# Kernel optimization log

Measured on AMD Instinct MI355X. Metric: run time of the kernel, lower is better.

The kernel has to match this reference:

```python
import jax, jax.numpy as jnp
import numpy as np
import math

B, D, NH, HD, FF, P, IMG = 4, 768, 12, 64, 3072, 16, 256
L = (IMG // P) ** 2      # 256 tokens
PD = P * P * 3           # 768 patch dim
GRID = IMG // P          # 16


def setup_inputs() -> dict:
    key = jax.random.key(0)
    ks = iter(jax.random.split(key, 80))
    def nrm(shape, s=0.02):
        return jax.random.normal(next(ks), shape, jnp.float32) * s
    return {
        "x": jax.random.normal(next(ks), (B, 3, IMG, IMG), jnp.float32),
        "pe_norm_w": jnp.ones((PD,), jnp.float32),
        "pe_proj_w": nrm((PD, D)),
        "pe_proj_b": jnp.zeros((D,), jnp.float32),
        "pe_norm_out_w": jnp.ones((D,), jnp.float32),
        "pos_embed": nrm((1, L, D)),
        "in_attn_norm_w": jnp.ones((6, D), jnp.float32),
        "in_qkv_w": nrm((6, D, 3 * D)),
        "in_out_w": nrm((6, D, D)),
        "in_ff_norm_w": jnp.ones((6, D), jnp.float32),
        "in_w1": nrm((6, D, 2 * FF)),
        "in_w2": nrm((6, FF, D)),
        "mid_attn_norm_w": jnp.ones((3, D), jnp.float32),
        "mid_qkv_w": nrm((3, D, 3 * D)),
        "mid_out_w": nrm((3, D, D)),
        "mid_ff_norm_w": jnp.ones((3, D), jnp.float32),
        "mid_w1": nrm((3, D, 2 * FF)),
        "mid_w2": nrm((3, FF, D)),
        "out_skip_w": nrm((2 * D, D)),
        "out_skip_b": jnp.zeros((D,), jnp.float32),
        "out_attn_norm_w": jnp.ones((D,), jnp.float32),
        "out_qkv_w": nrm((D, 3 * D)),
        "out_out_w": nrm((D, D)),
        "out_ff_norm_w": jnp.ones((D,), jnp.float32),
        "out_w1": nrm((D, 2 * FF)),
        "out_w2": nrm((FF, D)),
        "final_norm_w": jnp.ones((D,), jnp.float32),
        "ol_proj_w": nrm((D, PD)),
        "ol_proj_b": jnp.zeros((PD,), jnp.float32),
        "rb_conv_in_w": nrm((128, 3, 3, 3), 0.1),
        "rb_gn_w": jnp.ones((5, 128), jnp.float32),
        "rb_gn_b": jnp.zeros((5, 128), jnp.float32),
        "rb_conv1_w": nrm((128, 1, 5, 5), 0.1),
        "rb_conv2_w": nrm((128, 1, 5, 5), 0.1),
        "head_conv_w": nrm((1, 128, 3, 3), 0.1),
    }


def _mish(x):
    return x * jnp.tanh(jax.nn.softplus(x))


def _rms(x, w, eps=1e-5):
    return x * jax.lax.rsqrt(jnp.mean(x * x, axis=-1, keepdims=True) + eps) * w


def _attn(x, qkv_w, out_w):
    b, l, _ = x.shape
    q, k, v = jnp.split(x @ qkv_w, 3, axis=-1)
    s = 1.0 / math.sqrt(HD)  # applied to BOTH q and k, as in source
    q = (q * s).reshape(b, l, NH, HD)
    k = (k * s).reshape(b, l, NH, HD)
    v = v.reshape(b, l, NH, HD)
    logits = jnp.einsum('bqhd,bkhd->bhqk', q, k).astype(jnp.float32)
    w = jax.nn.softmax(logits, axis=-1).astype(x.dtype)
    o = jnp.einsum('bhqk,bkhd->bqhd', w, v).reshape(b, l, NH * HD)
    return o @ out_w


def _ff(x, w1, w2):
    a, g = jnp.split(x @ w1, 2, axis=-1)
    return (_mish(a) * g) @ w2


def _block(x, an, qkv, ow, fn, w1, w2):
    x = x + _attn(_rms(x, an), qkv, ow)
    x = x + _ff(_rms(x, fn), w1, w2)
    return x


def _gn(x, w, b, groups=8, eps=1e-5):
    bb, c, h, ww = x.shape
    xg = x.reshape(bb, groups, c // groups, h, ww)
    m = jnp.mean(xg, axis=(2, 3, 4), keepdims=True)
    v = jnp.var(xg, axis=(2, 3, 4), keepdims=True)
    xn = ((xg - m) * jax.lax.rsqrt(v + eps)).reshape(bb, c, h, ww)
    return xn * w[:, None, None] + b[:, None, None]


def _conv(x, w, pad, dil=1, groups=1):
    xp = jnp.pad(x, ((0, 0), (0, 0), (pad, pad), (pad, pad)), mode='reflect')
    return jax.lax.conv_general_dilated(
        xp, w, window_strides=(1, 1), padding='VALID', rhs_dilation=(dil, dil),
        feature_group_count=groups, dimension_numbers=('NCHW', 'OIHW', 'NCHW'))


def _forward(x, pe_norm_w, pe_proj_w, pe_proj_b, pe_norm_out_w, pos_embed,
             in_attn_norm_w, in_qkv_w, in_out_w, in_ff_norm_w, in_w1, in_w2,
             mid_attn_norm_w, mid_qkv_w, mid_out_w, mid_ff_norm_w, mid_w1, mid_w2,
             out_skip_w, out_skip_b, out_attn_norm_w, out_qkv_w, out_out_w,
             out_ff_norm_w, out_w1, out_w2, final_norm_w, ol_proj_w, ol_proj_b,
             rb_conv_in_w, rb_gn_w, rb_gn_b, rb_conv1_w, rb_conv2_w, head_conv_w):
    b = x.shape[0]
    # PatchEmbed: b c (h p1) (w p2) -> b (h w) (p1 p2 c)
    t = x.reshape(b, 3, GRID, P, GRID, P).transpose(0, 2, 4, 3, 5, 1).reshape(b, L, PD)
    t = _rms(t, pe_norm_w)
    t = t @ pe_proj_w + pe_proj_b
    t = _rms(t, pe_norm_out_w)
    t = t + pos_embed
    # U-ViT trunk: 6 in blocks (skips saved), 3 middle, 1 out block (source typo -> single out block)
    skips = []
    for i in range(6):
        t = _block(t, in_attn_norm_w[i], in_qkv_w[i], in_out_w[i],
                   in_ff_norm_w[i], in_w1[i], in_w2[i])
        skips.append(t)
    for i in range(3):
        t = _block(t, mid_attn_norm_w[i], mid_qkv_w[i], mid_out_w[i],
                   mid_ff_norm_w[i], mid_w1[i], mid_w2[i])
    t = jnp.concatenate([t, skips[-1]], axis=-1) @ out_skip_w + out_skip_b
    t = _block(t, out_attn_norm_w, out_qkv_w, out_out_w, out_ff_norm_w, out_w1, out_w2)
    t = _rms(t, final_norm_w)
    # OutBlock: proj, dropout(eval=identity), unpatchify to b 3 256 256
    t = t @ ol_proj_w + ol_proj_b
    img = t.reshape(b, GRID, GRID, P, P, 3).transpose(0, 5, 1, 3, 2, 4).reshape(b, 3, IMG, IMG)
    # ResNetBlock(128)
    h = _conv(img, rb_conv_in_w, 1)
    h = _mish(_gn(h, rb_gn_w[0], rb_gn_b[0]))
    res = h
    h = _mish(_gn(_conv(h, rb_conv1_w, 2, 1, 128), rb_gn_w[1], rb_gn_b[1]))
    h = res + h
    h = _mish(_gn(h, rb_gn_w[2], rb_gn_b[2]))
    res = h
    h = _mish(_gn(_conv(h, rb_conv2_w, 6, 3, 128), rb_gn_w[3], rb_gn_b[3]))
    h = res + h
    h = _mish(_gn(h, rb_gn_w[4], rb_gn_b[4]))
    return _conv(h, head_conv_w, 1)  # [B, 1, 256, 256]


def reference(x, pe_norm_w, pe_proj_w, pe_proj_b, pe_norm_out_w, pos_embed,
              in_attn_norm_w, in_qkv_w, in_out_w, in_ff_norm_w, in_w1, in_w2,
              mid_attn_norm_w, mid_qkv_w, mid_out_w, mid_ff_norm_w, mid_w1, mid_w2,
              out_skip_w, out_skip_b, out_attn_norm_w, out_qkv_w, out_out_w,
              out_ff_norm_w, out_w1, out_w2, final_norm_w, ol_proj_w, ol_proj_b,
              rb_conv_in_w, rb_gn_w, rb_gn_b, rb_conv1_w, rb_conv2_w, head_conv_w):
    return _forward(x, pe_norm_w, pe_proj_w, pe_proj_b, pe_norm_out_w, pos_embed,
                    in_attn_norm_w, in_qkv_w, in_out_w, in_ff_norm_w, in_w1, in_w2,
                    mid_attn_norm_w, mid_qkv_w, mid_out_w, mid_ff_norm_w, mid_w1, mid_w2,
                    out_skip_w, out_skip_b, out_attn_norm_w, out_qkv_w, out_out_w,
                    out_ff_norm_w, out_w1, out_w2, final_norm_w, ol_proj_w, ol_proj_b,
                    rb_conv_in_w, rb_gn_w, rb_gn_b, rb_conv1_w, rb_conv2_w, head_conv_w)
```

## Files before the change

### kernel.cpp

```cpp
#include <hip/hip_runtime.h>
#include <math.h>

#define B_ 4
#define D_ 768
#define NH_ 12
#define HD_ 64
#define FF_ 3072
#define L_ 256
#define PD_ 768
#define GRID_ 16
#define P_ 16
#define IMG_ 256
#define M_ (B_*L_)
#define NCONV_ (B_*128*IMG_*IMG_)

typedef __attribute__((ext_vector_type(8))) short short8;
typedef __attribute__((ext_vector_type(4))) float f32x4;
typedef __attribute__((ext_vector_type(4))) unsigned short us4;
typedef __attribute__((ext_vector_type(8))) unsigned short us8;
typedef unsigned short ushort_t;

__device__ __forceinline__ float mishf(float x){
    float e = __expf(x);
    float u = (1.f + e) * (1.f + e);
    return x * (1.f - 2.f / (u + 1.f));
}

__device__ __forceinline__ int refl(int i, int n){
    if (i < 0) i = -i;
    if (i >= n) i = 2*n - 2 - i;
    return i;
}

__device__ __forceinline__ ushort_t f2bf(float f){
    unsigned int u = __float_as_uint(f);
    unsigned int r = (u + 0x7FFFu + ((u >> 16) & 1u)) >> 16;
    return (ushort_t)r;
}
__device__ __forceinline__ float bf2f(ushort_t u){
    return __uint_as_float(((unsigned int)u) << 16);
}

__device__ __forceinline__ void gl16(const void* g, void* l){
    __builtin_amdgcn_global_load_lds(
        (const __attribute__((address_space(1))) unsigned int*)g,
        (__attribute__((address_space(3))) unsigned int*)l, 16, 0, 0);
}

__device__ __forceinline__ void block_red2(float& s, float& q){
    #pragma unroll
    for (int o = 32; o > 0; o >>= 1){ s += __shfl_down(s, o); q += __shfl_down(q, o); }
    __shared__ float r1[4], r2[4];
    int tid = threadIdx.x;
    if ((tid & 63) == 0){ r1[tid>>6] = s; r2[tid>>6] = q; }
    __syncthreads();
    if (tid == 0){ s = r1[0]+r1[1]+r1[2]+r1[3]; q = r2[0]+r2[1]+r2[2]+r2[3]; }
    __syncthreads();
}

__global__ __launch_bounds__(256) void k_patchify(const float* __restrict__ x, float* __restrict__ t){
    int idx = blockIdx.x*256 + threadIdx.x;
    int d = idx % PD_; int l = (idx/PD_) % L_; int b = idx/(PD_*L_);
    int c = d % 3; int p = d / 3; int p1 = p / P_; int p2 = p % P_;
    int gh = l / GRID_; int gw = l % GRID_;
    int sy = gh*P_ + p1, sx = gw*P_ + p2;
    t[idx] = x[(((size_t)b*3 + c)*IMG_ + sy)*IMG_ + sx];
}

__global__ __launch_bounds__(256) void k_wt(const float* __restrict__ b0, const float* __restrict__ b1,
                                            const float* __restrict__ b2, int n0, int n1,
                                            ushort_t* __restrict__ dst, int K, int N){
    int z = blockIdx.z;
    size_t sz = (size_t)K * N;
    const float* src = (z < n0) ? b0 + (size_t)z*sz
                     : (z < n0+n1) ? b1 + (size_t)(z-n0)*sz
                     : b2 + (size_t)(z-n0-n1)*sz;
    ushort_t* out = dst + (size_t)z*sz;
    __shared__ float ld[32][33];
    int k0 = blockIdx.y*32, nc0 = blockIdx.x*32;
    int tid = threadIdx.x;
    int c = tid & 31, r8 = tid >> 5;
    #pragma unroll
    for (int i = 0; i < 4; ++i){
        int k = r8 + i*8;
        ld[k][c] = src[(size_t)(k0+k)*N + nc0 + c];
    }
    __syncthreads();
    #pragma unroll
    for (int i = 0; i < 4; ++i){
        int n = r8 + i*8;
        out[(size_t)(nc0+n)*K + k0 + c] = f2bf(ld[c][n]);
    }
}

template<bool OUT_BF>
__global__ __launch_bounds__(256) void k_rms(const float* __restrict__ x, const float* __restrict__ w,
                                             const float* __restrict__ addv, void* __restrict__ yv){
    int row = blockIdx.x;
    const float* xr = x + (size_t)row * D_;
    float s = 0.f;
    for (int i = threadIdx.x; i < D_; i += 256){ float v = xr[i]; s += v*v; }
    __shared__ float red[256];
    red[threadIdx.x] = s; __syncthreads();
    for (int o = 128; o > 0; o >>= 1){
        if (threadIdx.x < o) red[threadIdx.x] += red[threadIdx.x+o];
        __syncthreads();
    }
    float rstd = rsqrtf(red[0]/(float)D_ + 1e-5f);
    int l = row % L_;
    for (int i = threadIdx.x; i < D_; i += 256){
        float v = xr[i]*rstd*w[i];
        if (addv) v += addv[(size_t)l*D_ + i];
        if (OUT_BF) ((ushort_t*)yv)[(size_t)row*D_ + i] = f2bf(v);
        else        ((float*)yv)[(size_t)row*D_ + i] = v;
    }
}

__global__ __launch_bounds__(256) void k_skred_rms(const float* __restrict__ Pp, float* __restrict__ t,
                                                   const float* __restrict__ w, ushort_t* __restrict__ nb){
    int row = blockIdx.x;
    int tid = threadIdx.x;
    float v[3];
    float s = 0.f;
    #pragma unroll
    for (int i = 0; i < 3; ++i){
        int c = tid + i*256;
        size_t o = (size_t)row*D_ + c;
        float x = t[o] + Pp[o] + Pp[(size_t)M_*D_ + o];
        v[i] = x; s += x*x;
        t[o] = x;
    }
    #pragma unroll
    for (int o = 32; o > 0; o >>= 1) s += __shfl_down(s, o);
    __shared__ float r1[4];
    if ((tid & 63) == 0) r1[tid>>6] = s;
    __syncthreads();
    float tot = r1[0]+r1[1]+r1[2]+r1[3];
    float rstd = rsqrtf(tot*(1.f/768.f) + 1e-5f);
    if (w){
        #pragma unroll
        for (int i = 0; i < 3; ++i){
            int c = tid + i*256;
            nb[(size_t)row*D_ + c] = f2bf(v[i]*rstd*w[c]);
        }
    }
}

template<bool OBF, int SPLITK>
__global__ __launch_bounds__(256) void k_gemm(const ushort_t* __restrict__ A, const ushort_t* __restrict__ Wt,
                                              void* __restrict__ Cv, const float* __restrict__ bias,
                                              const float* __restrict__ res, int N, int K){
    __shared__ ushort_t As[2][64][32];
    __shared__ ushort_t Ws[2][64][32];
    int tid = threadIdx.x;
    int lane = tid & 63, wid = tid >> 6;
    int wr = wid >> 1, wc = wid & 1;
    int row0 = blockIdx.y * 64, col0 = blockIdx.x * 64;
    f32x4 acc[2][2];
    #pragma unroll
    for (int i = 0; i < 2; ++i)
        #pragma unroll
        for (int j = 0; j < 2; ++j) acc[i][j] = (f32x4){0.f,0.f,0.f,0.f};

    int lg = lane >> 4, lr = lane & 15;
    int kc = K / SPLITK;
    int k0 = (SPLITK > 1) ? blockIdx.z * kc : 0;
    int srow = wid*16 + (lane >> 2);
    int scol = (lane & 3) * 8;
    const ushort_t* gA = A  + (size_t)(row0 + srow)*K + k0 + scol;
    const ushort_t* gW = Wt + (size_t)(col0 + srow)*K + k0 + scol;
    ushort_t* lA0 = &As[0][wid*16][0];
    ushort_t* lA1 = &As[1][wid*16][0];
    ushort_t* lW0 = &Ws[0][wid*16][0];
    ushort_t* lW1 = &Ws[1][wid*16][0];

    for (int kt = 0; kt < kc; kt += 64){
        __syncthreads();
        gl16(gA + kt,      lA0);
        gl16(gA + kt + 32, lA1);
        gl16(gW + kt,      lW0);
        gl16(gW + kt + 32, lW1);
        __syncthreads();
        short8 a0[2], a1[2], b0[2], b1[2];
        #pragma unroll
        for (int i = 0; i < 2; ++i){
            a0[i] = *(const short8*)(&As[0][wr*32 + i*16 + lr][lg*8]);
            a1[i] = *(const short8*)(&As[1][wr*32 + i*16 + lr][lg*8]);
        }
        #pragma unroll
        for (int j = 0; j < 2; ++j){
            b0[j] = *(const short8*)(&Ws[0][wc*32 + j*16 + lr][lg*8]);
            b1[j] = *(const short8*)(&Ws[1][wc*32 + j*16 + lr][lg*8]);
        }
        #pragma unroll
        for (int i = 0; i < 2; ++i)
            #pragma unroll
            for (int j = 0; j < 2; ++j){
                acc[i][j] = __builtin_amdgcn_mfma_f32_16x16x32_bf16(a0[i], b0[j], acc[i][j], 0, 0, 0);
                acc[i][j] = __builtin_amdgcn_mfma_f32_16x16x32_bf16(a1[i], b1[j], acc[i][j], 0, 0, 0);
            }
    }
    if (SPLITK > 1){
        float* Pp = (float*)Cv + (size_t)blockIdx.z * M_ * N;
        #pragma unroll
        for (int i = 0; i < 2; ++i)
            #pragma unroll
            for (int j = 0; j < 2; ++j)
                #pragma unroll
                for (int q = 0; q < 4; ++q){
                    int m = row0 + wr*32 + i*16 + lg*4 + q;
                    int n = col0 + wc*32 + j*16 + lr;
                    Pp[(size_t)m*N + n] = acc[i][j][q];
                }
    } else {
        #pragma unroll
        for (int i = 0; i < 2; ++i)
            #pragma unroll
            for (int j = 0; j < 2; ++j)
                #pragma unroll
                for (int q = 0; q < 4; ++q){
                    int m = row0 + wr*32 + i*16 + lg*4 + q;
                    int n = col0 + wc*32 + j*16 + lr;
                    float v = acc[i][j][q];
                    if (bias) v += bias[n];
                    size_t o = (size_t)m*N + n;
                    if (OBF){
                        ((ushort_t*)Cv)[o] = f2bf(v);
                    } else {
                        if (res) v += res[o];
                        ((float*)Cv)[o] = v;
                    }
                }
    }
}

__global__ __launch_bounds__(256) void k_gemm_glu(const ushort_t* __restrict__ A, const ushort_t* __restrict__ Wt,
                                                  ushort_t* __restrict__ Cb, int K){
    __shared__ ushort_t As[2][64][32];
    __shared__ ushort_t Wa[2][64][32];
    __shared__ ushort_t Wg[2][64][32];
    int tid = threadIdx.x;
    int lane = tid & 63, wid = tid >> 6;
    int wr = wid >> 1, wc = wid & 1;
    int row0 = blockIdx.y * 64, col0 = blockIdx.x * 64;
    f32x4 aa[2][2], ag[2][2];
    #pragma unroll
    for (int i = 0; i < 2; ++i)
        #pragma unroll
        for (int j = 0; j < 2; ++j){ aa[i][j] = (f32x4){0.f,0.f,0.f,0.f}; ag[i][j] = (f32x4){0.f,0.f,0.f,0.f}; }

    int lg = lane >> 4, lr = lane & 15;
    int srow = wid*16 + (lane >> 2);
    int scol = (lane & 3) * 8;
    const ushort_t* gA  = A  + (size_t)(row0 + srow)*K + scol;
    const ushort_t* gWa = Wt + (size_t)(col0 + srow)*K + scol;
    const ushort_t* gWg = Wt + (size_t)(FF_ + col0 + srow)*K + scol;
    ushort_t* lA0 = &As[0][wid*16][0];  ushort_t* lA1 = &As[1][wid*16][0];
    ushort_t* la0 = &Wa[0][wid*16][0];  ushort_t* la1 = &Wa[1][wid*16][0];
    ushort_t* lg0 = &Wg[0][wid*16][0];  ushort_t* lg1 = &Wg[1][wid*16][0];

    for (int kt = 0; kt < K; kt += 64){
        __syncthreads();
        gl16(gA  + kt,      lA0);
        gl16(gA  + kt + 32, lA1);
        gl16(gWa + kt,      la0);
        gl16(gWa + kt + 32, la1);
        gl16(gWg + kt,      lg0);
        gl16(gWg + kt + 32, lg1);
        __syncthreads();
        short8 a0[2], a1[2], ba0[2], ba1[2], bg0[2], bg1[2];
        #pragma unroll
        for (int i = 0; i < 2; ++i){
            a0[i] = *(const short8*)(&As[0][wr*32 + i*16 + lr][lg*8]);
            a1[i] = *(const short8*)(&As[1][wr*32 + i*16 + lr][lg*8]);
        }
        #pragma unroll
        for (int j = 0; j < 2; ++j){
            ba0[j] = *(const short8*)(&Wa[0][wc*32 + j*16 + lr][lg*8]);
            ba1[j] = *(const short8*)(&Wa[1][wc*32 + j*16 + lr][lg*8]);
            bg0[j] = *(const short8*)(&Wg[0][wc*32 + j*16 + lr][lg*8]);
            bg1[j] = *(const short8*)(&Wg[1][wc*32 + j*16 + lr][lg*8]);
        }
        #pragma unroll
        for (int i = 0; i < 2; ++i)
            #pragma unroll
            for (int j = 0; j < 2; ++j){
                aa[i][j] = __builtin_amdgcn_mfma_f32_16x16x32_bf16(a0[i], ba0[j], aa[i][j], 0, 0, 0);
                aa[i][j] = __builtin_amdgcn_mfma_f32_16x16x32_bf16(a1[i], ba1[j], aa[i][j], 0, 0, 0);
                ag[i][j] = __builtin_amdgcn_mfma_f32_16x16x32_bf16(a0[i], bg0[j], ag[i][j], 0, 0, 0);
                ag[i][j] = __builtin_amdgcn_mfma_f32_16x16x32_bf16(a1[i], bg1[j], ag[i][j], 0, 0, 0);
            }
    }
    #pragma unroll
    for (int i = 0; i < 2; ++i)
        #pragma unroll
        for (int j = 0; j < 2; ++j)
            #pragma unroll
            for (int q = 0; q < 4; ++q){
                int m = row0 + wr*32 + i*16 + lg*4 + q;
                int n = col0 + wc*32 + j*16 + lr;
                Cb[(size_t)m*FF_ + n] = f2bf(mishf(aa[i][j][q]) * ag[i][j][q]);
            }
}

__global__ __launch_bounds__(256) void k_attn(const ushort_t* __restrict__ qkv, ushort_t* __restrict__ out){
    int qt = blockIdx.x, h = blockIdx.y, b = blockIdx.z;
    const ushort_t* base = qkv + (size_t)b * L_ * 3 * D_;
    __shared__ ushort_t Qs[64][72];
    __shared__ ushort_t KVs[64][72];
    __shared__ ushort_t Ps[64][268];
    __shared__ float red[8][64];
    int tid = threadIdx.x;
    int lane = tid & 63, w = tid >> 6;
    int lr = lane & 15, lg = lane >> 4;

    {
        int r = tid >> 2, c = (tid & 3) * 16;
        const ushort_t* src = base + (size_t)(qt*64 + r)*3*D_ + h*HD_ + c;
        *(us8*)&Qs[r][c]   = *(const us8*)src;
        *(us8*)&Qs[r][c+8] = *(const us8*)(src + 8);
    }

    f32x4 sacc[4][4];
    #pragma unroll
    for (int kt = 0; kt < 4; ++kt)
        #pragma unroll
        for (int mi = 0; mi < 4; ++mi) sacc[kt][mi] = (f32x4){0.f,0.f,0.f,0.f};

    for (int kt = 0; kt < 4; ++kt){
        __syncthreads();
        {
            int r = tid >> 2, c = (tid & 3) * 16;
            const ushort_t* src = base + (size_t)(kt*64 + r)*3*D_ + D_ + h*HD_ + c;
            *(us8*)&KVs[r][c]   = *(const us8*)src;
            *(us8*)&KVs[r][c+8] = *(const us8*)(src + 8);
        }
        __syncthreads();
        short8 bk0 = *(const short8*)&KVs[w*16 + lr][lg*8];
        short8 bk1 = *(const short8*)&KVs[w*16 + lr][32 + lg*8];
        #pragma unroll
        for (int mi = 0; mi < 4; ++mi){
            short8 a0 = *(const short8*)&Qs[mi*16 + lr][lg*8];
            short8 a1 = *(const short8*)&Qs[mi*16 + lr][32 + lg*8];
            sacc[kt][mi] = __builtin_amdgcn_mfma_f32_16x16x32_bf16(a0, bk0, sacc[kt][mi], 0, 0, 0);
            sacc[kt][mi] = __builtin_amdgcn_mfma_f32_16x16x32_bf16(a1, bk1, sacc[kt][mi], 0, 0, 0);
        }
    }

    const float inv64 = 1.0f/64.0f;
    float gm[4][4], linv[4][4];
    #pragma unroll
    for (int mi = 0; mi < 4; ++mi){
        #pragma unroll
        for (int r = 0; r < 4; ++r){
            float v = fmaxf(fmaxf(sacc[0][mi][r], sacc[1][mi][r]), fmaxf(sacc[2][mi][r], sacc[3][mi][r]));
            v = fmaxf(v, __shfl_xor(v, 1));
            v = fmaxf(v, __shfl_xor(v, 2));
            v = fmaxf(v, __shfl_xor(v, 4));
            v = fmaxf(v, __shfl_xor(v, 8));
            gm[mi][r] = v;
            if (lr == 0) red[w][mi*16 + lg*4 + r] = v;
        }
    }
    __syncthreads();
    #pragma unroll
    for (int mi = 0; mi < 4; ++mi){
        #pragma unroll
        for (int r = 0; r < 4; ++r){
            int row = mi*16 + lg*4 + r;
            float m = fmaxf(fmaxf(red[0][row], red[1][row]), fmaxf(red[2][row], red[3][row]));
            gm[mi][r] = m;
            float sum = 0.f;
            #pragma unroll
            for (int kt = 0; kt < 4; ++kt){
                float p = __expf((sacc[kt][mi][r] - m) * inv64);
                Ps[row][kt*64 + w*16 + lr] = f2bf(p);
                sum += p;
            }
            sum += __shfl_xor(sum, 1);
            sum += __shfl_xor(sum, 2);
            sum += __shfl_xor(sum, 4);
            sum += __shfl_xor(sum, 8);
            linv[mi][r] = sum;
            if (lr == 0) red[4 + w][row] = sum;
        }
    }
    __syncthreads();
    #pragma unroll
    for (int mi = 0; mi < 4; ++mi){
        #pragma unroll
        for (int r = 0; r < 4; ++r){
            int row = mi*16 + lg*4 + r;
            linv[mi][r] = 1.0f / (red[4][row] + red[5][row] + red[6][row] + red[7][row]);
        }
    }

    f32x4 oacc[4];
    #pragma unroll
    for (int mi = 0; mi < 4; ++mi) oacc[mi] = (f32x4){0.f,0.f,0.f,0.f};
    for (int kt = 0; kt < 4; ++kt){
        __syncthreads();
        {
            int k = tid & 63, dg = tid >> 6;
            const ushort_t* src = base + (size_t)(kt*64 + k)*3*D_ + 2*D_ + h*HD_ + dg*16;
            us8 v0 = *(const us8*)src;
            us8 v1 = *(const us8*)(src + 8);
            #pragma unroll
            for (int j = 0; j < 8; ++j) KVs[dg*16 + j][k] = v0[j];
            #pragma unroll
            for (int j = 0; j < 8; ++j) KVs[dg*16 + 8 + j][k] = v1[j];
        }
        __syncthreads();
        short8 bv0 = *(const short8*)&KVs[w*16 + lr][lg*8];
        short8 bv1 = *(const short8*)&KVs[w*16 + lr][32 + lg*8];
        #pragma unroll
        for (int mi = 0; mi < 4; ++mi){
            short8 a0 = *(const short8*)&Ps[mi*16 + lr][kt*64 + lg*8];
            short8 a1 = *(const short8*)&Ps[mi*16 + lr][kt*64 + 32 + lg*8];
            oacc[mi] = __builtin_amdgcn_mfma_f32_16x16x32_bf16(a0, bv0, oacc[mi], 0, 0, 0);
            oacc[mi] = __builtin_amdgcn_mfma_f32_16x16x32_bf16(a1, bv1, oacc[mi], 0, 0, 0);
        }
    }
    #pragma unroll
    for (int mi = 0; mi < 4; ++mi){
        #pragma unroll
        for (int r = 0; r < 4; ++r){
            int row = mi*16 + lg*4 + r;
            out[((size_t)(b*L_ + qt*64 + row))*D_ + h*HD_ + w*16 + lr] = f2bf(oacc[mi][r] * linv[mi][r]);
        }
    }
}

__global__ __launch_bounds__(256) void k_cat(const float* __restrict__ t, const float* __restrict__ skip,
                                             ushort_t* __restrict__ cat){
    int i4 = (blockIdx.x*256 + threadIdx.x) * 4;
    int r = i4 / D_, c = i4 % D_;
    float4 a = *(const float4*)(t + i4);
    float4 b = *(const float4*)(skip + i4);
    us4 ua, ub;
    ua.x=f2bf(a.x); ua.y=f2bf(a.y); ua.z=f2bf(a.z); ua.w=f2bf(a.w);
    ub.x=f2bf(b.x); ub.y=f2bf(b.y); ub.z=f2bf(b.z); ub.w=f2bf(b.w);
    *(us4*)(cat + (size_t)r*1536 + c) = ua;
    *(us4*)(cat + (size_t)r*1536 + 768 + c) = ub;
}

__global__ __launch_bounds__(256) void k_unpatchify(const float* __restrict__ t, float* __restrict__ img){
    int idx = blockIdx.x*256 + threadIdx.x;
    int sx = idx % IMG_; int sy = (idx/IMG_)%IMG_; int c = (idx/(IMG_*IMG_))%3; int b = idx/(3*IMG_*IMG_);
    int gh = sy / P_, p1 = sy % P_, gw = sx / P_, p2 = sx % P_;
    img[idx] = t[(((size_t)b*L_) + gh*GRID_+gw)*PD_ + (p1*P_+p2)*3 + c];
}

__global__ __launch_bounds__(256) void k_conv_in(const float* __restrict__ img, const float* __restrict__ w,
                                                 ushort_t* __restrict__ out, float* __restrict__ partial){
    int y = blockIdx.x, ocg = blockIdx.y, b = blockIdx.z;
    int x = threadIdx.x;
    __shared__ float rows[9][IMG_];
    int yy0 = refl(y-1, IMG_), yy2 = refl(y+1, IMG_);
    #pragma unroll
    for (int ic = 0; ic < 3; ++ic){
        const float* basep = img + ((size_t)(b*3+ic))*IMG_*IMG_;
        rows[ic*3+0][x] = basep[(size_t)yy0*IMG_ + x];
        rows[ic*3+1][x] = basep[(size_t)y  *IMG_ + x];
        rows[ic*3+2][x] = basep[(size_t)yy2*IMG_ + x];
    }
    __syncthreads();
    int xl = (x==0)?1:x-1, xr = (x==255)?254:x+1;
    float sg = 0.f, qg = 0.f;
    for (int oc = ocg*32; oc < ocg*32 + 32; ++oc){
        const float* wv = w + oc*27;
        float acc = 0.f;
        #pragma unroll
        for (int ic = 0; ic < 3; ++ic){
            const float* wk = wv + ic*9;
            acc += rows[ic*3+0][xl]*wk[0] + rows[ic*3+0][x]*wk[1] + rows[ic*3+0][xr]*wk[2]
                 + rows[ic*3+1][xl]*wk[3] + rows[ic*3+1][x]*wk[4] + rows[ic*3+1][xr]*wk[5]
                 + rows[ic*3+2][xl]*wk[6] + rows[ic*3+2][x]*wk[7] + rows[ic*3+2][xr]*wk[8];
        }
        out[(((size_t)(b*128+oc))*IMG_ + y)*IMG_ + x] = f2bf(acc);
        sg += acc; qg += acc*acc;
        if ((oc & 15) == 15){
            block_red2(sg, qg);
            if (threadIdx.x == 0){
                int pidx = ((b*8 + (oc>>4))*256 + y);
                partial[pidx*2] = sg; partial[pidx*2+1] = qg;
            }
            sg = 0.f; qg = 0.f;
        }
    }
}

__global__ __launch_bounds__(256) void k_gn_fin(const float* __restrict__ partial, int nper,
                                                float* __restrict__ stats){
    int bg = blockIdx.x, tid = threadIdx.x;
    float s = 0.f, q = 0.f;
    for (int i = tid; i < nper; i += 256){
        s += partial[((size_t)bg*nper + i)*2];
        q += partial[((size_t)bg*nper + i)*2 + 1];
    }
    block_red2(s, q);
    if (tid == 0){
        const float n = 16.f*IMG_*IMG_;
        float m = s/n;
        float var = q/n - m*m;
        stats[bg*2]   = m;
        stats[bg*2+1] = rsqrtf(var + 1e-5f);
    }
}

__global__ __launch_bounds__(256) void k_act(const ushort_t* __restrict__ x, const float* __restrict__ st,
                                             const float* __restrict__ gw, const float* __restrict__ gb,
                                             ushort_t* __restrict__ y){
    int bid = blockIdx.x;
    int b = bid >> 11, c = (bid >> 4) & 127;
    int bg = b*8 + (c>>4);
    float sc = st[bg*2+1]*gw[c], sb = gb[c] - st[bg*2]*sc;
    size_t e0 = (size_t)bid*4096 + threadIdx.x*16;
    us8 v0 = *(const us8*)(x + e0), v1 = *(const us8*)(x + e0 + 8);
    us8 r0, r1;
    #pragma unroll
    for (int i = 0; i < 8; ++i) r0[i] = f2bf(mishf(bf2f(v0[i])*sc + sb));
    #pragma unroll
    for (int i = 0; i < 8; ++i) r1[i] = f2bf(mishf(bf2f(v1[i])*sc + sb));
    *(us8*)(y + e0) = r0;
    *(us8*)(y + e0 + 8) = r1;
}

template<int PAD, int DIL>
__global__ __launch_bounds__(256) void k_dw(const ushort_t* __restrict__ in,
                                            const float* __restrict__ cw,
                                            ushort_t* __restrict__ out, float* __restrict__ partial){
    constexpr int AP = (DIL==1) ? 4 : 8;
    constexpr int SC = (DIL==1) ? 40 : 48;
    constexpr int SY = 64 + 2*PAD;
    constexpr int CH = SC/4;
    __shared__ float tile[SY*SC];
    int tileid = blockIdx.x, c = blockIdx.y, b = blockIdx.z;
    int x0 = (tileid & 7) * 32, y0 = (tileid >> 3) * 64;
    int tid = threadIdx.x;
    const ushort_t* ip = in + ((size_t)(b*128+c))*IMG_*IMG_;
    int xs = x0 - AP;
    if (xs >= 0 && xs + SC <= IMG_){
        for (int j = tid; j < SY*CH; j += 256){
            int r = j / CH, q = j - r*CH;
            int gy = refl(y0 - PAD + r, IMG_);
            us4 v = *(const us4*)(ip + (size_t)gy*IMG_ + xs + q*4);
            f32x4 fv = { bf2f(v.x), bf2f(v.y), bf2f(v.z), bf2f(v.w) };
            *(f32x4*)&tile[r*SC + q*4] = fv;
        }
    } else {
        for (int j = tid; j < SY*SC; j += 256){
            int r = j / SC, cc = j - r*SC;
            int gy = refl(y0 - PAD + r, IMG_);
            int gx = refl(xs + cc, IMG_);
            tile[r*SC + cc] = bf2f(ip[(size_t)gy*IMG_ + gx]);
        }
    }
    __syncthreads();
    float wreg[25];
    #pragma unroll
    for (int u = 0; u < 25; ++u) wreg[u] = cw[c*25 + u];
    int tx4 = (tid & 7)*4, ty = tid >> 3;
    constexpr int NV = (DIL==1) ? 3 : 5;
    float s = 0.f, q2 = 0.f;
    #pragma unroll
    for (int rr = 0; rr < 2; ++rr){
        int yy = ty + rr*32;
        float acc[4] = {0.f,0.f,0.f,0.f};
        #pragma unroll
        for (int kh = 0; kh < 5; ++kh){
            const float* rowp = &tile[(yy + kh*DIL)*SC + tx4];
            float vv[NV*4];
            #pragma unroll
            for (int u = 0; u < NV; ++u){
                f32x4 v = *(const f32x4*)(rowp + u*4);
                vv[u*4]=v.x; vv[u*4+1]=v.y; vv[u*4+2]=v.z; vv[u*4+3]=v.w;
            }
            #pragma unroll
            for (int kw = 0; kw < 5; ++kw){
                float wk = wreg[kh*5+kw];
                #pragma unroll
                for (int j = 0; j < 4; ++j)
                    acc[j] += vv[kw*DIL + j + (AP - 2*DIL)] * wk;
            }
        }
        us4 o4 = { f2bf(acc[0]), f2bf(acc[1]), f2bf(acc[2]), f2bf(acc[3]) };
        *(us4*)(out + (((size_t)(b*128+c))*IMG_ + y0+yy)*IMG_ + x0+tx4) = o4;
        s  += acc[0]+acc[1]+acc[2]+acc[3];
        q2 += acc[0]*acc[0]+acc[1]*acc[1]+acc[2]*acc[2]+acc[3]*acc[3];
    }
    block_red2(s, q2);
    if (tid == 0){
        int bid = (b*128 + c)*32 + tileid;
        partial[bid*2] = s; partial[bid*2+1] = q2;
    }
}

__global__ __launch_bounds__(256) void k_addmish(const ushort_t* __restrict__ xn, const float* __restrict__ stn,
                                                 const float* __restrict__ wn, const float* __restrict__ bn,
                                                 const ushort_t* __restrict__ resa,
                                                 ushort_t* __restrict__ out, float* __restrict__ partial){
    int bid = blockIdx.x;
    int b = bid >> 11, c = (bid >> 4) & 127;
    int bg = b*8 + (c>>4);
    float scn = stn[bg*2+1]*wn[c], sbn = bn[c] - stn[bg*2]*scn;
    size_t e0 = (size_t)bid*4096 + threadIdx.x*16;
    us8 vn0 = *(const us8*)(xn + e0), vn1 = *(const us8*)(xn + e0 + 8);
    us8 vr0 = *(const us8*)(resa + e0), vr1 = *(const us8*)(resa + e0 + 8);
    us8 r0, r1;
    float s = 0.f, q = 0.f;
    #pragma unroll
    for (int i = 0; i < 8; ++i){
        float v = mishf(bf2f(vn0[i])*scn + sbn) + bf2f(vr0[i]);
        s += v; q += v*v; r0[i] = f2bf(v);
    }
    #pragma unroll
    for (int i = 0; i < 8; ++i){
        float v = mishf(bf2f(vn1[i])*scn + sbn) + bf2f(vr1[i]);
        s += v; q += v*v; r1[i] = f2bf(v);
    }
    *(us8*)(out + e0) = r0;
    *(us8*)(out + e0 + 8) = r1;
    block_red2(s, q);
    if (threadIdx.x == 0){ partial[bid*2] = s; partial[bid*2+1] = q; }
}

__global__ __launch_bounds__(256) void k_head_part(const ushort_t* __restrict__ in, const float* __restrict__ st,
                                                   const float* __restrict__ gw, const float* __restrict__ gb,
                                                   const float* __restrict__ w, float* __restrict__ part){
    __shared__ float tile[34*34];
    int tileid = blockIdx.x, cg = blockIdx.y, b = blockIdx.z;
    int x0 = (tileid & 7)*32, y0 = (tileid >> 3)*32;
    int tid = threadIdx.x;
    int tx4 = (tid & 7)*4, ty = tid >> 3;
    float m  = st[(b*8+cg)*2];
    float rs = st[(b*8+cg)*2 + 1];
    float acc[4] = {0.f,0.f,0.f,0.f};
    for (int ci = 0; ci < 16; ++ci){
        int c = cg*16 + ci;
        float sc = rs*gw[c], sb = gb[c] - m*sc;
        const ushort_t* ip = in + ((size_t)(b*128+c))*IMG_*IMG_;
        if (ci) __syncthreads();
        for (int i = tid; i < 34*34; i += 256){
            int r = i/34, cc = i - r*34;
            int gy = refl(y0-1+r, IMG_);
            int gx = refl(x0-1+cc, IMG_);
            tile[i] = mishf(bf2f(ip[(size_t)gy*IMG_+gx])*sc + sb);
        }
        __syncthreads();
        const float* wc = w + c*9;
        #pragma unroll
        for (int kh = 0; kh < 3; ++kh){
            float vv[6];
            #pragma unroll
            for (int u = 0; u < 6; ++u) vv[u] = tile[(ty+kh)*34 + tx4 + u];
            #pragma unroll
            for (int kw = 0; kw < 3; ++kw){
                float wk = wc[kh*3+kw];
                #pragma unroll
                for (int j = 0; j < 4; ++j) acc[j] += vv[kw+j]*wk;
            }
        }
    }
    f32x4 o = {acc[0], acc[1], acc[2], acc[3]};
    *(f32x4*)(part + (((size_t)(cg*4+b))*IMG_ + y0+ty)*IMG_ + x0+tx4) = o;
}

__global__ __launch_bounds__(256) void k_head_fin(const float* __restrict__ part, float* __restrict__ out){
    int idx4 = blockIdx.x*256 + threadIdx.x;
    size_t e = (size_t)idx4*4;
    int b = (int)(e / (IMG_*IMG_));
    size_t off = e % (IMG_*IMG_);
    f32x4 s = {0.f,0.f,0.f,0.f};
    #pragma unroll
    for (int cg = 0; cg < 8; ++cg){
        f32x4 v = *(const f32x4*)(part + (size_t)(cg*4+b)*IMG_*IMG_ + off);
        s.x += v.x; s.y += v.y; s.z += v.z; s.w += v.w;
    }
    *(f32x4*)(out + e) = s;
}


struct WsMap {
    float *t, *skip, *t2, *ybuf, *img, *partial, *hpart, *stats, *part;
    ushort_t *nb, *qkvb, *ab, *gbuf, *cat, *wb_qkv, *wb_out, *wb_w1, *wb_w2, *wb_pe, *wb_skip, *wb_ol, *cA, *cB;
};

static void run_block(const float* fn, const ushort_t* qw, const ushort_t* ow,
                      const ushort_t* w1, const ushort_t* w2, const float* next_w,
                      float* t, const WsMap& W, hipStream_t stream){
    k_gemm<true,1><<<dim3(3*D_/64, M_/64), 256, 0, stream>>>(W.nb, qw, W.qkvb, nullptr, nullptr, 3*D_, D_);
    k_attn<<<dim3(4, NH_, B_), 256, 0, stream>>>(W.qkvb, W.ab);
    k_gemm<false,2><<<dim3(D_/64, M_/64, 2), 256, 0, stream>>>(W.ab, ow, W.part, nullptr, nullptr, D_, D_);
    k_skred_rms<<<M_, 256, 0, stream>>>(W.part, t, fn, W.nb);
    k_gemm_glu<<<dim3(FF_/64, M_/64), 256, 0, stream>>>(W.nb, w1, W.gbuf, D_);
    k_gemm<false,2><<<dim3(D_/64, M_/64, 2), 256, 0, stream>>>(W.gbuf, w2, W.part, nullptr, nullptr, D_, FF_);
    k_skred_rms<<<M_, 256, 0, stream>>>(W.part, t, next_w, W.nb);
}

extern "C" void kernel_launch(void* const* d_in, const int* in_sizes, int n_in,
                              void* d_out, int out_size, void* d_ws, size_t ws_size,
                              hipStream_t stream){
    const float* x              = (const float*)d_in[0];
    const float* pe_norm_w      = (const float*)d_in[1];
    const float* pe_proj_w      = (const float*)d_in[2];
    const float* pe_proj_b      = (const float*)d_in[3];
    const float* pe_norm_out_w  = (const float*)d_in[4];
    const float* pos_embed      = (const float*)d_in[5];
    const float* in_attn_norm_w = (const float*)d_in[6];
    const float* in_qkv_w       = (const float*)d_in[7];
    const float* in_out_w       = (const float*)d_in[8];
    const float* in_ff_norm_w   = (const float*)d_in[9];
    const float* in_w1          = (const float*)d_in[10];
    const float* in_w2          = (const float*)d_in[11];
    const float* mid_attn_norm_w= (const float*)d_in[12];
    const float* mid_qkv_w      = (const float*)d_in[13];
    const float* mid_out_w      = (const float*)d_in[14];
    const float* mid_ff_norm_w  = (const float*)d_in[15];
    const float* mid_w1         = (const float*)d_in[16];
    const float* mid_w2         = (const float*)d_in[17];
    const float* out_skip_w     = (const float*)d_in[18];
    const float* out_skip_b     = (const float*)d_in[19];
    const float* out_attn_norm_w= (const float*)d_in[20];
    const float* out_qkv_w      = (const float*)d_in[21];
    const float* out_out_w      = (const float*)d_in[22];
    const float* out_ff_norm_w  = (const float*)d_in[23];
    const float* out_w1         = (const float*)d_in[24];
    const float* out_w2         = (const float*)d_in[25];
    const float* final_norm_w   = (const float*)d_in[26];
    const float* ol_proj_w      = (const float*)d_in[27];
    const float* ol_proj_b      = (const float*)d_in[28];
    const float* rb_conv_in_w   = (const float*)d_in[29];
    const float* rb_gn_w        = (const float*)d_in[30];
    const float* rb_gn_b        = (const float*)d_in[31];
    const float* rb_conv1_w     = (const float*)d_in[32];
    const float* rb_conv2_w     = (const float*)d_in[33];
    const float* head_conv_w    = (const float*)d_in[34];

    WsMap W;
    float* f = (float*)d_ws;
    const size_t TD = (size_t)M_*D_;
    W.t      = f;               f += TD;
    W.skip   = f;               f += TD;
    W.t2     = f;               f += TD;
    W.ybuf   = f;               f += TD;
    W.img    = f;               f += TD;
    W.partial= f;               f += 131072;
    W.hpart  = f;               f += (size_t)8*4*IMG_*IMG_;
    W.stats  = f;               f += 448;
    W.part   = f;               f += (size_t)4*TD;
    ushort_t* u = (ushort_t*)f;
    W.nb     = u;               u += TD;
    W.qkvb   = u;               u += (size_t)M_*3*D_;
    W.ab     = u;               u += TD;
    W.gbuf   = u;               u += (size_t)M_*FF_;
    W.cat    = u;               u += (size_t)M_*2*D_;
    W.wb_qkv = u;               u += (size_t)10*D_*3*D_;
    W.wb_out = u;               u += (size_t)10*D_*D_;
    W.wb_w1  = u;               u += (size_t)10*D_*2*FF_;
    W.wb_w2  = u;               u += (size_t)10*FF_*D_;
    W.wb_pe  = u;               u += (size_t)D_*D_;
    W.wb_skip= u;               u += (size_t)2*D_*D_;
    W.wb_ol  = u;               u += (size_t)D_*D_;
    W.cA     = u;               u += (size_t)NCONV_;
    W.cB     = u;

    float* st0 = W.stats;       float* st1 = W.stats + 64;
    float* st2 = W.stats + 128; float* st3 = W.stats + 192;
    float* st4 = W.stats + 256;

    k_wt<<<dim3(3*D_/32, D_/32, 10), 256, 0, stream>>>(in_qkv_w, mid_qkv_w, out_qkv_w, 6, 3, W.wb_qkv, D_, 3*D_);
    k_wt<<<dim3(D_/32, D_/32, 10), 256, 0, stream>>>(in_out_w, mid_out_w, out_out_w, 6, 3, W.wb_out, D_, D_);
    k_wt<<<dim3(2*FF_/32, D_/32, 10), 256, 0, stream>>>(in_w1, mid_w1, out_w1, 6, 3, W.wb_w1, D_, 2*FF_);
    k_wt<<<dim3(D_/32, FF_/32, 10), 256, 0, stream>>>(in_w2, mid_w2, out_w2, 6, 3, W.wb_w2, FF_, D_);
    k_wt<<<dim3(D_/32, D_/32, 1), 256, 0, stream>>>(pe_proj_w, nullptr, nullptr, 1, 0, W.wb_pe, D_, D_);
    k_wt<<<dim3(D_/32, 2*D_/32, 1), 256, 0, stream>>>(out_skip_w, nullptr, nullptr, 1, 0, W.wb_skip, 2*D_, D_);
    k_wt<<<dim3(D_/32, D_/32, 1), 256, 0, stream>>>(ol_proj_w, nullptr, nullptr, 1, 0, W.wb_ol, D_, D_);

    k_patchify<<<(B_*L_*PD_)/256, 256, 0, stream>>>(x, W.t2);
    k_rms<true><<<M_, 256, 0, stream>>>(W.t2, pe_norm_w, nullptr, W.nb);
    k_gemm<false,1><<<dim3(D_/64, M_/64), 256, 0, stream>>>(W.nb, W.wb_pe, W.t, pe_proj_b, nullptr, D_, D_);
    k_rms<false><<<M_, 256, 0, stream>>>(W.t, pe_norm_out_w, pos_embed, W.t);
    k_rms<true><<<M_, 256, 0, stream>>>(W.t, in_attn_norm_w, nullptr, W.nb);

    for (int i = 0; i < 6; ++i){
        const float* next_w = (i < 5) ? in_attn_norm_w + (size_t)(i+1)*D_ : mid_attn_norm_w;
        run_block(in_ff_norm_w + (size_t)i*D_, W.wb_qkv + (size_t)i*D_*3*D_,
                  W.wb_out + (size_t)i*D_*D_,
                  W.wb_w1 + (size_t)i*D_*2*FF_, W.wb_w2 + (size_t)i*FF_*D_,
                  next_w, W.t, W, stream);
    }
    hipMemcpyAsync(W.skip, W.t, TD*sizeof(float), hipMemcpyDeviceToDevice, stream);

    for (int i = 0; i < 3; ++i){
        int z = 6 + i;
        const float* next_w = (i < 2) ? mid_attn_norm_w + (size_t)(i+1)*D_ : nullptr;
        run_block(mid_ff_norm_w + (size_t)i*D_, W.wb_qkv + (size_t)z*D_*3*D_,
                  W.wb_out + (size_t)z*D_*D_,
                  W.wb_w1 + (size_t)z*D_*2*FF_, W.wb_w2 + (size_t)z*FF_*D_,
                  next_w, W.t, W, stream);
    }

    k_cat<<<(M_*D_)/1024, 256, 0, stream>>>(W.t, W.skip, W.cat);
    k_gemm<false,1><<<dim3(D_/64, M_/64), 256, 0, stream>>>(W.cat, W.wb_skip, W.t2, out_skip_b, nullptr, D_, 2*D_);

    k_rms<true><<<M_, 256, 0, stream>>>(W.t2, out_attn_norm_w, nullptr, W.nb);
    run_block(out_ff_norm_w, W.wb_qkv + (size_t)9*D_*3*D_, W.wb_out + (size_t)9*D_*D_,
              W.wb_w1 + (size_t)9*D_*2*FF_, W.wb_w2 + (size_t)9*FF_*D_,
              final_norm_w, W.t2, W, stream);

    k_gemm<false,1><<<dim3(PD_/64, M_/64), 256, 0, stream>>>(W.nb, W.wb_ol, W.ybuf, ol_proj_b, nullptr, PD_, D_);
    k_unpatchify<<<(B_*3*IMG_*IMG_)/256, 256, 0, stream>>>(W.ybuf, W.img);

    k_conv_in<<<dim3(256, 4, 4), 256, 0, stream>>>(W.img, rb_conv_in_w, W.cA, W.partial);
    k_gn_fin<<<32, 256, 0, stream>>>(W.partial, 256, st0);
    k_act<<<8192, 256, 0, stream>>>(W.cA, st0, rb_gn_w, rb_gn_b, W.cB);
    k_dw<2,1><<<dim3(32, 128, 4), 256, 0, stream>>>(W.cB, rb_conv1_w, W.cA, W.partial);
    k_gn_fin<<<32, 256, 0, stream>>>(W.partial, 512, st1);
    k_addmish<<<8192, 256, 0, stream>>>(W.cA, st1, rb_gn_w+128, rb_gn_b+128, W.cB, W.cA, W.partial);
    k_gn_fin<<<32, 256, 0, stream>>>(W.partial, 256, st2);
    k_act<<<8192, 256, 0, stream>>>(W.cA, st2, rb_gn_w+256, rb_gn_b+256, W.cB);
    k_dw<6,3><<<dim3(32, 128, 4), 256, 0, stream>>>(W.cB, rb_conv2_w, W.cA, W.partial);
    k_gn_fin<<<32, 256, 0, stream>>>(W.partial, 512, st3);
    k_addmish<<<8192, 256, 0, stream>>>(W.cA, st3, rb_gn_w+384, rb_gn_b+384, W.cB, W.cA, W.partial);
    k_gn_fin<<<32, 256, 0, stream>>>(W.partial, 256, st4);
    k_head_part<<<dim3(64, 8, 4), 256, 0, stream>>>(W.cA, st4, rb_gn_w+512, rb_gn_b+512, head_conv_w, W.hpart);
    k_head_fin<<<(B_*IMG_*IMG_)/1024, 256, 0, stream>>>(W.hpart, (float*)d_out);
}
```

Measured before the change: 1.417 ms.

## Double-buffer LDS tiles with prefetch in GEMM and gated-FF GEMM kernels

Both MFMA GEMM kernels now load the first K tile before the loop and, on each iteration, start the global-to-LDS load of the next tile into the alternate buffer before computing on the current one. This leaves one barrier per iteration instead of two and lets global loads overlap with MFMA work. The plain GEMM doubles its LDS footprint to hold two 64-wide K stages. The gated GEMM keeps its LDS size but reuses the two halves as ping-pong buffers, so its K step drops from 64 to 32. That means more iterations and barriers there, and occupancy may fall for the plain GEMM.

```diff
diff --git a/kernel.cpp b/kernel.cpp
--- a/kernel.cpp
+++ b/kernel.cpp
@@ -150,8 +150,8 @@
 __global__ __launch_bounds__(256) void k_gemm(const ushort_t* __restrict__ A, const ushort_t* __restrict__ Wt,
                                               void* __restrict__ Cv, const float* __restrict__ bias,
                                               const float* __restrict__ res, int N, int K){
-    __shared__ ushort_t As[2][64][32];
-    __shared__ ushort_t Ws[2][64][32];
+    __shared__ ushort_t As[2][2][64][32];
+    __shared__ ushort_t Ws[2][2][64][32];
     int tid = threadIdx.x;
     int lane = tid & 63, wid = tid >> 6;
     int wr = wid >> 1, wc = wid & 1;
@@ -169,28 +169,31 @@
     int scol = (lane & 3) * 8;
     const ushort_t* gA = A  + (size_t)(row0 + srow)*K + k0 + scol;
     const ushort_t* gW = Wt + (size_t)(col0 + srow)*K + k0 + scol;
-    ushort_t* lA0 = &As[0][wid*16][0];
-    ushort_t* lA1 = &As[1][wid*16][0];
-    ushort_t* lW0 = &Ws[0][wid*16][0];
-    ushort_t* lW1 = &Ws[1][wid*16][0];
+
+    gl16(gA,      &As[0][0][wid*16][0]);
+    gl16(gA + 32, &As[0][1][wid*16][0]);
+    gl16(gW,      &Ws[0][0][wid*16][0]);
+    gl16(gW + 32, &Ws[0][1][wid*16][0]);
+    int cur = 0;
 
     for (int kt = 0; kt < kc; kt += 64){
         __syncthreads();
-        gl16(gA + kt,      lA0);
-        gl16(gA + kt + 32, lA1);
-        gl16(gW + kt,      lW0);
-        gl16(gW + kt + 32, lW1);
-        __syncthreads();
+        if (kt + 64 < kc){
+            gl16(gA + kt + 64, &As[cur^1][0][wid*16][0]);
+            gl16(gA + kt + 96, &As[cur^1][1][wid*16][0]);
+            gl16(gW + kt + 64, &Ws[cur^1][0][wid*16][0]);
+            gl16(gW + kt + 96, &Ws[cur^1][1][wid*16][0]);
+        }
         short8 a0[2], a1[2], b0[2], b1[2];
         #pragma unroll
         for (int i = 0; i < 2; ++i){
-            a0[i] = *(const short8*)(&As[0][wr*32 + i*16 + lr][lg*8]);
-            a1[i] = *(const short8*)(&As[1][wr*32 + i*16 + lr][lg*8]);
+            a0[i] = *(const short8*)(&As[cur][0][wr*32 + i*16 + lr][lg*8]);
+            a1[i] = *(const short8*)(&As[cur][1][wr*32 + i*16 + lr][lg*8]);
         }
         #pragma unroll
         for (int j = 0; j < 2; ++j){
-            b0[j] = *(const short8*)(&Ws[0][wc*32 + j*16 + lr][lg*8]);
-            b1[j] = *(const short8*)(&Ws[1][wc*32 + j*16 + lr][lg*8]);
+            b0[j] = *(const short8*)(&Ws[cur][0][wc*32 + j*16 + lr][lg*8]);
+            b1[j] = *(const short8*)(&Ws[cur][1][wc*32 + j*16 + lr][lg*8]);
         }
         #pragma unroll
         for (int i = 0; i < 2; ++i)
@@ -199,6 +202,7 @@
                 acc[i][j] = __builtin_amdgcn_mfma_f32_16x16x32_bf16(a0[i], b0[j], acc[i][j], 0, 0, 0);
                 acc[i][j] = __builtin_amdgcn_mfma_f32_16x16x32_bf16(a1[i], b1[j], acc[i][j], 0, 0, 0);
             }
+        cur ^= 1;
     }
     if (SPLITK > 1){
         float* Pp = (float*)Cv + (size_t)blockIdx.z * M_ * N;
@@ -255,41 +259,35 @@
     const ushort_t* gA  = A  + (size_t)(row0 + srow)*K + scol;
     const ushort_t* gWa = Wt + (size_t)(col0 + srow)*K + scol;
     const ushort_t* gWg = Wt + (size_t)(FF_ + col0 + srow)*K + scol;
-    ushort_t* lA0 = &As[0][wid*16][0];  ushort_t* lA1 = &As[1][wid*16][0];
-    ushort_t* la0 = &Wa[0][wid*16][0];  ushort_t* la1 = &Wa[1][wid*16][0];
-    ushort_t* lg0 = &Wg[0][wid*16][0];  ushort_t* lg1 = &Wg[1][wid*16][0];
-
-    for (int kt = 0; kt < K; kt += 64){
+
+    gl16(gA,  &As[0][wid*16][0]);
+    gl16(gWa, &Wa[0][wid*16][0]);
+    gl16(gWg, &Wg[0][wid*16][0]);
+    int cur = 0;
+
+    for (int kt = 0; kt < K; kt += 32){
         __syncthreads();
-        gl16(gA  + kt,      lA0);
-        gl16(gA  + kt + 32, lA1);
-        gl16(gWa + kt,      la0);
-        gl16(gWa + kt + 32, la1);
-        gl16(gWg + kt,      lg0);
-        gl16(gWg + kt + 32, lg1);
-        __syncthreads();
-        short8 a0[2], a1[2], ba0[2], ba1[2], bg0[2], bg1[2];
-        #pragma unroll
-        for (int i = 0; i < 2; ++i){
-            a0[i] = *(const short8*)(&As[0][wr*32 + i*16 + lr][lg*8]);
-            a1[i] = *(const short8*)(&As[1][wr*32 + i*16 + lr][lg*8]);
-        }
+        if (kt + 32 < K){
+            gl16(gA  + kt + 32, &As[cur^1][wid*16][0]);
+            gl16(gWa + kt + 32, &Wa[cur^1][wid*16][0]);
+            gl16(gWg + kt + 32, &Wg[cur^1][wid*16][0]);
+        }
+        short8 a[2], ba[2], bg[2];
+        #pragma unroll
+        for (int i = 0; i < 2; ++i) a[i] = *(const short8*)(&As[cur][wr*32 + i*16 + lr][lg*8]);
         #pragma unroll
         for (int j = 0; j < 2; ++j){
-            ba0[j] = *(const short8*)(&Wa[0][wc*32 + j*16 + lr][lg*8]);
-            ba1[j] = *(const short8*)(&Wa[1][wc*32 + j*16 + lr][lg*8]);
-            bg0[j] = *(const short8*)(&Wg[0][wc*32 + j*16 + lr][lg*8]);
-            bg1[j] = *(const short8*)(&Wg[1][wc*32 + j*16 + lr][lg*8]);
+            ba[j] = *(const short8*)(&Wa[cur][wc*32 + j*16 + lr][lg*8]);
+            bg[j] = *(const short8*)(&Wg[cur][wc*32 + j*16 + lr][lg*8]);
         }
         #pragma unroll
         for (int i = 0; i < 2; ++i)
             #pragma unroll
             for (int j = 0; j < 2; ++j){
-                aa[i][j] = __builtin_amdgcn_mfma_f32_16x16x32_bf16(a0[i], ba0[j], aa[i][j], 0, 0, 0);
-                aa[i][j] = __builtin_amdgcn_mfma_f32_16x16x32_bf16(a1[i], ba1[j], aa[i][j], 0, 0, 0);
-                ag[i][j] = __builtin_amdgcn_mfma_f32_16x16x32_bf16(a0[i], bg0[j], ag[i][j], 0, 0, 0);
-                ag[i][j] = __builtin_amdgcn_mfma_f32_16x16x32_bf16(a1[i], bg1[j], ag[i][j], 0, 0, 0);
+                aa[i][j] = __builtin_amdgcn_mfma_f32_16x16x32_bf16(a[i], ba[j], aa[i][j], 0, 0, 0);
+                ag[i][j] = __builtin_amdgcn_mfma_f32_16x16x32_bf16(a[i], bg[j], ag[i][j], 0, 0, 0);
             }
+        cur ^= 1;
     }
     #pragma unroll
     for (int i = 0; i < 2; ++i)
```

New measurement: 1.449 ms. 2.3% more time.
